# Kernel tuning notes

Measured on AMD Instinct MI355X. Metric: run time of the kernel, lower is better.

Reference implementation:

```python
import jax, jax.numpy as jnp
import numpy as np

N, E, D, OUT = 50000, 800000, 64, 64
NEG_INF = jnp.float32(-1e30)


def _masked_edge_softmax(logits, mask, dst, n):
    # softmax over incoming edges of each dst node, restricted to mask
    l = jnp.where(mask, logits, NEG_INF)
    m = jax.ops.segment_max(l, dst, num_segments=n)        # [N]
    m = jnp.maximum(m, NEG_INF)                            # empty segments -> -1e30
    e = jnp.where(mask, jnp.exp(l - m[dst]), jnp.float32(0.0))  # [E]
    s = jax.ops.segment_sum(e, dst, num_segments=n)        # [N]
    return e / (s[dst] + jnp.float32(1e-16))               # [E]


def setup_inputs() -> dict:
    key = jax.random.key(0)
    ks = jax.random.split(key, 6)
    feat = jax.random.normal(ks[0], (N, D), dtype=jnp.float32)
    w = jax.random.normal(ks[1], (E,), dtype=jnp.float32)
    src = jax.random.randint(ks[2], (E,), 0, N, dtype=jnp.int32)
    dst = jax.random.randint(ks[3], (E,), 0, N, dtype=jnp.int32)
    # xavier_uniform with relu gain on fc weight
    gain = np.sqrt(2.0)
    limit = np.float32(gain * np.sqrt(6.0 / (3 * D + OUT)))
    W_fc = jax.random.uniform(ks[4], (OUT, 3 * D), jnp.float32, -limit, limit)
    b_fc = jnp.zeros((OUT,), jnp.float32)
    bias = jnp.zeros((OUT,), jnp.float32)
    return {
        "feat": feat, "w": w, "W_fc": W_fc, "b_fc": b_fc, "bias": bias,
        "coef_self": jnp.ones((1,), jnp.float32),
        "coef_posi": jnp.ones((1,), jnp.float32),
        "coef_nega": jnp.ones((1,), jnp.float32),
        "src": src, "dst": dst,
    }


def reference(feat, w, W_fc, b_fc, bias, coef_self, coef_posi, coef_nega, src, dst):
    n = feat.shape[0]
    pos_mask = w > 0
    neg_mask = w < 0
    # edge softmax over signed subgraphs (negative subgraph uses |w|)
    a_pos = _masked_edge_softmax(w, pos_mask, dst, n)              # [E]
    a_neg = _masked_edge_softmax(jnp.abs(w), neg_mask, dst, n)     # [E]
    # u_mul_e -> sum aggregation: gather source feats, weight, scatter to dst
    src_feat = feat[src]                                           # [E, D]
    h_pos = jax.ops.segment_sum(src_feat * a_pos[:, None], dst, num_segments=n)
    h_neg = jax.ops.segment_sum(src_feat * a_neg[:, None], dst, num_segments=n)
    feat_combined = jnp.concatenate(
        [coef_self * feat, coef_posi * h_pos, coef_nega * h_neg], axis=1)  # [N, 3D]
    rst = feat_combined @ W_fc.T + b_fc + bias
    return rst
```

## Files before the change

kernel.cpp:

```cpp
#include <hip/hip_runtime.h>

#define D 64
#define K3 192
#define OUTD 64
#define KPB 512
#define KPB_LOG 9
#define NBMAX 256
#define ABATCH 4096
#define CAP 8192

typedef __attribute__((ext_vector_type(8))) short bf16x8;
typedef __attribute__((ext_vector_type(4))) float f32x4;

static __device__ __forceinline__ unsigned short f2bf(float f) {
    unsigned u = __float_as_uint(f);
    u += 0x7fffu + ((u >> 16) & 1u);
    return (unsigned short)(u >> 16);
}

__global__ void build_bfrag_kernel(const float* __restrict__ W_fc,
                                   unsigned short* __restrict__ Bfrag,
                                   int* __restrict__ cursorA, int NB) {
    int i = blockIdx.x * blockDim.x + threadIdx.x;
    if (i < NB) cursorA[i] = i * CAP;
    if (i >= 6 * 4 * 64 * 8) return;
    int j    = i & 7;
    int lane = (i >> 3) & 63;
    int nt   = (i >> 9) & 3;
    int kt   = i >> 11;
    int n = nt * 16 + (lane & 15);
    int k = kt * 32 + (lane >> 4) * 8 + j;
    Bfrag[i] = f2bf(W_fc[n * K3 + k]);
}

__global__ __launch_bounds__(256) void bin_kernel(
        const float* __restrict__ w, const int* __restrict__ src,
        const int* __restrict__ dst, int* __restrict__ cursorA,
        uint2* __restrict__ staged, int E, int NB) {
    __shared__ int cnt[NBMAX];
    __shared__ int base[NBMAX];
    int t = threadIdx.x;
    int e0 = blockIdx.x * ABATCH;
    for (int i = t; i < NB; i += 256) cnt[i] = 0;
    __syncthreads();

    unsigned wv[16], yv[16];
    int bk[16], rk[16];
#pragma unroll
    for (int j = 0; j < 16; ++j) {
        int e = e0 + j * 256 + t;
        if (e < E) {
            float we = w[e];
            int key = 2 * dst[e] + (we < 0.0f ? 1 : 0);
            wv[j] = __float_as_uint(we);
            yv[j] = ((unsigned)src[e] << KPB_LOG) | (unsigned)(key & (KPB - 1));
            bk[j] = key >> KPB_LOG;
            rk[j] = atomicAdd(&cnt[bk[j]], 1);
        } else {
            bk[j] = -1;
        }
    }
    __syncthreads();
    for (int b = t; b < NB; b += 256) {
        int c = cnt[b];
        if (c > 0) base[b] = atomicAdd(&cursorA[b], c);
    }
    __syncthreads();
#pragma unroll
    for (int j = 0; j < 16; ++j) {
        if (bk[j] >= 0) {
            int pos = base[bk[j]] + rk[j];
            if (pos < (bk[j] + 1) * CAP)
                staged[pos] = make_uint2(wv[j], yv[j]);
        }
    }
}

__global__ __launch_bounds__(256) void bucket_scatter_kernel(
        const int* __restrict__ cursorA, const uint2* __restrict__ staged,
        int2* __restrict__ seg_be, uint2* __restrict__ e_pack, int M) {
    __shared__ int cnt[KPB];
    __shared__ int wt[4];
    int b = blockIdx.x;
    int t = threadIdx.x;
    int lane = t & 63;
    int wid = t >> 6;
    int kb = b << KPB_LOG;
    int nk = min(KPB, M - kb);
    int beg = b * CAP;
    int end = min(cursorA[b], beg + CAP);

    cnt[2 * t] = 0;
    cnt[2 * t + 1] = 0;
    __syncthreads();
    for (int i = beg + t; i < end; i += 256)
        atomicAdd(&cnt[staged[i].y & (KPB - 1)], 1);
    __syncthreads();

    int v0 = cnt[2 * t], v1 = cnt[2 * t + 1];
    int ps = v0 + v1;
    int incl = ps;
#pragma unroll
    for (int o = 1; o < 64; o <<= 1) {
        int u = __shfl_up(incl, o);
        if (lane >= o) incl += u;
    }
    if (lane == 63) wt[wid] = incl;
    __syncthreads();
    int wb = 0;
    for (int j = 0; j < wid; ++j) wb += wt[j];
    int excl = wb + (incl - ps);

    int p0 = beg + excl;
    int p1 = p0 + v0;
    if (2 * t < nk) seg_be[kb + 2 * t] = make_int2(p0, p1);
    if (2 * t + 1 < nk) seg_be[kb + 2 * t + 1] = make_int2(p1, p1 + v1);
    __syncthreads();
    cnt[2 * t] = p0;
    cnt[2 * t + 1] = p1;
    __syncthreads();

    for (int i = beg + t; i < end; i += 256) {
        uint2 r = staged[i];
        int kl = (int)(r.y & (KPB - 1));
        int p = atomicAdd(&cnt[kl], 1);
        e_pack[p] = make_uint2(r.x, r.y >> KPB_LOG);
    }
}

__global__ __launch_bounds__(256) void node_agg_kernel(
        const float* __restrict__ feat,
        const int2* __restrict__ seg_be,
        const uint2* __restrict__ e_pack,
        float* __restrict__ h_pos,
        float* __restrict__ h_neg, int N) {
    int lane = threadIdx.x & 63;
    int seg = (blockIdx.x * blockDim.x + threadIdx.x) >> 6;
    if (seg >= 2 * N) return;
    int2 be = seg_be[seg];
    int beg = __builtin_amdgcn_readfirstlane(be.x);
    int end = __builtin_amdgcn_readfirstlane(be.y);
    int isneg = seg & 1;

    float s = 0.0f, acc = 0.0f;
    if (isneg) {
#pragma unroll 4
        for (int e = beg; e < end; ++e) {
            uint2 pk = e_pack[e];
            float ws = __uint_as_float(pk.x);
            float aj = __expf(-ws);
            s += aj;
            acc = fmaf(feat[(size_t)(int)pk.y * D + lane], aj, acc);
        }
    } else {
#pragma unroll 4
        for (int e = beg; e < end; ++e) {
            uint2 pk = e_pack[e];
            float ws = __uint_as_float(pk.x);
            float aj = (ws > 0.0f) ? __expf(ws) : 0.0f;
            s += aj;
            acc = fmaf(feat[(size_t)(int)pk.y * D + lane], aj, acc);
        }
    }
    float r = acc / (s + 1e-16f);
    float* h = isneg ? h_neg : h_pos;
    h[(size_t)(seg >> 1) * D + lane] = r;
}

__global__ __launch_bounds__(256) void out_gemm_mfma(
        const float* __restrict__ feat,
        const float* __restrict__ h_pos,
        const float* __restrict__ h_neg,
        const unsigned short* __restrict__ Bfrag,
        const float* __restrict__ b_fc,
        const float* __restrict__ bias,
        const float* __restrict__ coef_self,
        const float* __restrict__ coef_posi,
        const float* __restrict__ coef_nega,
        float* __restrict__ out,
        int N) {
    int lane = threadIdx.x & 63;
    int wv = (blockIdx.x * blockDim.x + threadIdx.x) >> 6;
    int node0 = wv * 16;
    if (node0 >= N) return;

    const bf16x8* bp = (const bf16x8*)Bfrag;
    bf16x8 bfr[24];
#pragma unroll
    for (int f = 0; f < 24; ++f) bfr[f] = bp[f * 64 + lane];

    float cf[3];
    cf[0] = coef_self[0];
    cf[1] = coef_posi[0];
    cf[2] = coef_nega[0];
    const float* segs[3];
    segs[0] = feat;
    segs[1] = h_pos;
    segs[2] = h_neg;

    int m = lane & 15;
    int kg = lane >> 4;
    int node = node0 + m;
    bool mvalid = node < N;

    f32x4 acc[4];
#pragma unroll
    for (int nt = 0; nt < 4; ++nt) acc[nt] = (f32x4){0.f, 0.f, 0.f, 0.f};

#pragma unroll
    for (int kt = 0; kt < 6; ++kt) {
        int sg = kt >> 1;
        float c = cf[sg];
        const float* srcp = segs[sg] + (size_t)node * D + (kt & 1) * 32 + kg * 8;
        float v[8];
        if (mvalid) {
            float4 v0 = *(const float4*)(srcp);
            float4 v1 = *(const float4*)(srcp + 4);
            v[0] = v0.x; v[1] = v0.y; v[2] = v0.z; v[3] = v0.w;
            v[4] = v1.x; v[5] = v1.y; v[6] = v1.z; v[7] = v1.w;
        } else {
#pragma unroll
            for (int j = 0; j < 8; ++j) v[j] = 0.f;
        }
        bf16x8 a;
#pragma unroll
        for (int j = 0; j < 8; ++j) a[j] = (short)f2bf(v[j] * c);
#pragma unroll
        for (int nt = 0; nt < 4; ++nt)
            acc[nt] = __builtin_amdgcn_mfma_f32_16x16x32_bf16(
                a, bfr[kt * 4 + nt], acc[nt], 0, 0, 0);
    }

#pragma unroll
    for (int nt = 0; nt < 4; ++nt) {
        int col = nt * 16 + m;
        float bb = b_fc[col] + bias[col];
#pragma unroll
        for (int j = 0; j < 4; ++j) {
            int row = node0 + 4 * kg + j;
            if (row < N) out[(size_t)row * OUTD + col] = acc[nt][j] + bb;
        }
    }
}

extern "C" void kernel_launch(void* const* d_in, const int* in_sizes, int n_in,
                              void* d_out, int out_size, void* d_ws, size_t ws_size,
                              hipStream_t stream) {
    const float* feat      = (const float*)d_in[0];
    const float* w         = (const float*)d_in[1];
    const float* W_fc      = (const float*)d_in[2];
    const float* b_fc      = (const float*)d_in[3];
    const float* bias      = (const float*)d_in[4];
    const float* coef_self = (const float*)d_in[5];
    const float* coef_posi = (const float*)d_in[6];
    const float* coef_nega = (const float*)d_in[7];
    const int*   src       = (const int*)d_in[8];
    const int*   dst       = (const int*)d_in[9];

    const int E = in_sizes[1];
    const int N = in_sizes[0] / D;
    const int M = 2 * N;
    const int NB = (M + KPB - 1) / KPB;

    char* ws = (char*)d_ws;
    int2*  seg_be   = (int2*)ws;
    int*   cursorA  = (int*)(ws + (size_t)M * 8);
    size_t bfrag_off = (((size_t)M * 8 + (size_t)NB * 4) + 15) & ~(size_t)15;
    unsigned short* Bfrag = (unsigned short*)(ws + bfrag_off);
    size_t epack_off = (bfrag_off + 6 * 4 * 64 * 8 * 2 + 7) & ~(size_t)7;
    uint2* e_pack   = (uint2*)(ws + epack_off);
    float* h_pos    = (float*)(ws + epack_off + (size_t)NB * CAP * 8);
    float* h_neg    = h_pos + (size_t)N * D;
    uint2* staged   = (uint2*)h_pos;

    build_bfrag_kernel<<<(6 * 4 * 64 * 8 + 255) / 256, 256, 0, stream>>>(
        W_fc, Bfrag, cursorA, NB);
    bin_kernel<<<(E + ABATCH - 1) / ABATCH, 256, 0, stream>>>(
        w, src, dst, cursorA, staged, E, NB);
    bucket_scatter_kernel<<<NB, 256, 0, stream>>>(cursorA, staged, seg_be,
                                                  e_pack, M);

    int segb = (M * 64 + 255) / 256;
    node_agg_kernel<<<segb, 256, 0, stream>>>(feat, seg_be, e_pack, h_pos, h_neg, N);

    int nwaves = (N + 15) / 16;
    int gb = (nwaves + 3) / 4;
    out_gemm_mfma<<<gb, 256, 0, stream>>>(feat, h_pos, h_neg, Bfrag, b_fc, bias,
                                          coef_self, coef_posi, coef_nega,
                                          (float*)d_out, N);
}
```

Before: 89.62 us.

## Store features and aggregates in bf16 and fold coefficients into weight fragments

Adds a prep kernel that converts the node features to bf16 once and folds the three scalar coefficients into the bf16 weight fragments. The node aggregation then gathers bf16 features and writes bf16 h_pos/h_neg, and the GEMM loads bf16x8 operands directly instead of converting fp32. This halves the bytes moved by the random feature gather and by the GEMM input reads. It costs an extra full pass over the features and loses some precision in the aggregated values, which were previously fp32 before the GEMM rounded them. The workspace layout changes so staged no longer aliases h_pos.

```diff
diff --git a/kernel.cpp b/kernel.cpp
--- a/kernel.cpp
+++ b/kernel.cpp
@@ -17,20 +17,40 @@
     u += 0x7fffu + ((u >> 16) & 1u);
     return (unsigned short)(u >> 16);
 }
-
-__global__ void build_bfrag_kernel(const float* __restrict__ W_fc,
-                                   unsigned short* __restrict__ Bfrag,
-                                   int* __restrict__ cursorA, int NB) {
+static __device__ __forceinline__ float bf2f(unsigned short h) {
+    return __uint_as_float((unsigned)h << 16);
+}
+
+__global__ __launch_bounds__(256) void prep_kernel(
+        const float* __restrict__ W_fc,
+        const float* __restrict__ coef_self,
+        const float* __restrict__ coef_posi,
+        const float* __restrict__ coef_nega,
+        const float* __restrict__ feat,
+        unsigned short* __restrict__ Bfrag,
+        unsigned short* __restrict__ feat16,
+        int* __restrict__ cursorA, int NB, int ND4) {
     int i = blockIdx.x * blockDim.x + threadIdx.x;
     if (i < NB) cursorA[i] = i * CAP;
-    if (i >= 6 * 4 * 64 * 8) return;
-    int j    = i & 7;
-    int lane = (i >> 3) & 63;
-    int nt   = (i >> 9) & 3;
-    int kt   = i >> 11;
-    int n = nt * 16 + (lane & 15);
-    int k = kt * 32 + (lane >> 4) * 8 + j;
-    Bfrag[i] = f2bf(W_fc[n * K3 + k]);
+    if (i < 6 * 4 * 64 * 8) {
+        int j    = i & 7;
+        int lane = (i >> 3) & 63;
+        int nt   = (i >> 9) & 3;
+        int kt   = i >> 11;
+        int n = nt * 16 + (lane & 15);
+        int k = kt * 32 + (lane >> 4) * 8 + j;
+        float cf = (k < 64) ? coef_self[0] : (k < 128 ? coef_posi[0] : coef_nega[0]);
+        Bfrag[i] = f2bf(W_fc[n * K3 + k] * cf);
+    }
+    if (i < ND4) {
+        float4 v = *(const float4*)&feat[(size_t)i * 4];
+        unsigned long long p =
+            (unsigned long long)f2bf(v.x) |
+            ((unsigned long long)f2bf(v.y) << 16) |
+            ((unsigned long long)f2bf(v.z) << 32) |
+            ((unsigned long long)f2bf(v.w) << 48);
+        *(unsigned long long*)&feat16[(size_t)i * 4] = p;
+    }
 }
 
 __global__ __launch_bounds__(256) void bin_kernel(
@@ -129,11 +149,11 @@
 }
 
 __global__ __launch_bounds__(256) void node_agg_kernel(
-        const float* __restrict__ feat,
+        const unsigned short* __restrict__ feat16,
         const int2* __restrict__ seg_be,
         const uint2* __restrict__ e_pack,
-        float* __restrict__ h_pos,
-        float* __restrict__ h_neg, int N) {
+        unsigned short* __restrict__ h_pos,
+        unsigned short* __restrict__ h_neg, int N) {
     int lane = threadIdx.x & 63;
     int seg = (blockIdx.x * blockDim.x + threadIdx.x) >> 6;
     if (seg >= 2 * N) return;
@@ -150,7 +170,8 @@
             float ws = __uint_as_float(pk.x);
             float aj = __expf(-ws);
             s += aj;
-            acc = fmaf(feat[(size_t)(int)pk.y * D + lane], aj, acc);
+            float fv = bf2f(feat16[(size_t)(int)pk.y * D + lane]);
+            acc = fmaf(fv, aj, acc);
         }
     } else {
 #pragma unroll 4
@@ -159,24 +180,22 @@
             float ws = __uint_as_float(pk.x);
             float aj = (ws > 0.0f) ? __expf(ws) : 0.0f;
             s += aj;
-            acc = fmaf(feat[(size_t)(int)pk.y * D + lane], aj, acc);
+            float fv = bf2f(feat16[(size_t)(int)pk.y * D + lane]);
+            acc = fmaf(fv, aj, acc);
         }
     }
     float r = acc / (s + 1e-16f);
-    float* h = isneg ? h_neg : h_pos;
-    h[(size_t)(seg >> 1) * D + lane] = r;
+    unsigned short* h = isneg ? h_neg : h_pos;
+    h[(size_t)(seg >> 1) * D + lane] = f2bf(r);
 }
 
 __global__ __launch_bounds__(256) void out_gemm_mfma(
-        const float* __restrict__ feat,
-        const float* __restrict__ h_pos,
-        const float* __restrict__ h_neg,
+        const unsigned short* __restrict__ feat16,
+        const unsigned short* __restrict__ h_pos,
+        const unsigned short* __restrict__ h_neg,
         const unsigned short* __restrict__ Bfrag,
         const float* __restrict__ b_fc,
         const float* __restrict__ bias,
-        const float* __restrict__ coef_self,
-        const float* __restrict__ coef_posi,
-        const float* __restrict__ coef_nega,
         float* __restrict__ out,
         int N) {
     int lane = threadIdx.x & 63;
@@ -189,12 +208,8 @@
 #pragma unroll
     for (int f = 0; f < 24; ++f) bfr[f] = bp[f * 64 + lane];
 
-    float cf[3];
-    cf[0] = coef_self[0];
-    cf[1] = coef_posi[0];
-    cf[2] = coef_nega[0];
-    const float* segs[3];
-    segs[0] = feat;
+    const unsigned short* segs[3];
+    segs[0] = feat16;
     segs[1] = h_pos;
     segs[2] = h_neg;
 
@@ -210,21 +225,12 @@
 #pragma unroll
     for (int kt = 0; kt < 6; ++kt) {
         int sg = kt >> 1;
-        float c = cf[sg];
-        const float* srcp = segs[sg] + (size_t)node * D + (kt & 1) * 32 + kg * 8;
-        float v[8];
+        bf16x8 a;
         if (mvalid) {
-            float4 v0 = *(const float4*)(srcp);
-            float4 v1 = *(const float4*)(srcp + 4);
-            v[0] = v0.x; v[1] = v0.y; v[2] = v0.z; v[3] = v0.w;
-            v[4] = v1.x; v[5] = v1.y; v[6] = v1.z; v[7] = v1.w;
+            a = *(const bf16x8*)(segs[sg] + (size_t)node * D + (kt & 1) * 32 + kg * 8);
         } else {
-#pragma unroll
-            for (int j = 0; j < 8; ++j) v[j] = 0.f;
-        }
-        bf16x8 a;
-#pragma unroll
-        for (int j = 0; j < 8; ++j) a[j] = (short)f2bf(v[j] * c);
+            a = (bf16x8){0, 0, 0, 0, 0, 0, 0, 0};
+        }
 #pragma unroll
         for (int nt = 0; nt < 4; ++nt)
             acc[nt] = __builtin_amdgcn_mfma_f32_16x16x32_bf16(
@@ -267,25 +273,29 @@
     int*   cursorA  = (int*)(ws + (size_t)M * 8);
     size_t bfrag_off = (((size_t)M * 8 + (size_t)NB * 4) + 15) & ~(size_t)15;
     unsigned short* Bfrag = (unsigned short*)(ws + bfrag_off);
-    size_t epack_off = (bfrag_off + 6 * 4 * 64 * 8 * 2 + 7) & ~(size_t)7;
-    uint2* e_pack   = (uint2*)(ws + epack_off);
-    float* h_pos    = (float*)(ws + epack_off + (size_t)NB * CAP * 8);
-    float* h_neg    = h_pos + (size_t)N * D;
-    uint2* staged   = (uint2*)h_pos;
-
-    build_bfrag_kernel<<<(6 * 4 * 64 * 8 + 255) / 256, 256, 0, stream>>>(
-        W_fc, Bfrag, cursorA, NB);
+    size_t feat16_off = bfrag_off + 6 * 4 * 64 * 8 * 2;
+    unsigned short* feat16 = (unsigned short*)(ws + feat16_off);
+    size_t epack_off = (feat16_off + (size_t)N * D * 2 + 7) & ~(size_t)7;
+    uint2* e_pack  = (uint2*)(ws + epack_off);
+    uint2* staged  = e_pack + (size_t)NB * CAP;
+    unsigned short* h_pos = (unsigned short*)((char*)(staged + (size_t)NB * CAP));
+    unsigned short* h_neg = h_pos + (size_t)N * D;
+
+    const int ND4 = N * D / 4;
+    int pb = (max(ND4, 6 * 4 * 64 * 8) + 255) / 256;
+    prep_kernel<<<pb, 256, 0, stream>>>(W_fc, coef_self, coef_posi, coef_nega,
+                                        feat, Bfrag, feat16, cursorA, NB, ND4);
     bin_kernel<<<(E + ABATCH - 1) / ABATCH, 256, 0, stream>>>(
         w, src, dst, cursorA, staged, E, NB);
     bucket_scatter_kernel<<<NB, 256, 0, stream>>>(cursorA, staged, seg_be,
                                                   e_pack, M);
 
     int segb = (M * 64 + 255) / 256;
-    node_agg_kernel<<<segb, 256, 0, stream>>>(feat, seg_be, e_pack, h_pos, h_neg, N);
+    node_agg_kernel<<<segb, 256, 0, stream>>>(feat16, seg_be, e_pack,
+                                              h_pos, h_neg, N);
 
     int nwaves = (N + 15) / 16;
     int gb = (nwaves + 3) / 4;
-    out_gemm_mfma<<<gb, 256, 0, stream>>>(feat, h_pos, h_neg, Bfrag, b_fc, bias,
-                                          coef_self, coef_posi, coef_nega,
-                                          (float*)d_out, N);
-}
+    out_gemm_mfma<<<gb, 256, 0, stream>>>(feat16, h_pos, h_neg, Bfrag,
+                                          b_fc, bias, (float*)d_out, N);
+}
```

New measurement: 84.78 us. -5.4%, faster.
